# Performance work log

Hardware: AMD Instinct MI355X
Metric: run time of the kernel (lower is better)

The kernel has to match this reference:

```python
import jax, jax.numpy as jnp
import numpy as np

B, T, H, D = 4, 2048, 2048, 4
FF = 4 * H


def _ln(x, s, b):
    m = jnp.mean(x, axis=-1, keepdims=True)
    v = jnp.mean(jnp.square(x - m), axis=-1, keepdims=True)
    return (x - m) * jax.lax.rsqrt(v + 1e-5) * s + b


def setup_inputs() -> dict:
    key = jax.random.key(0)
    ks = jax.random.split(key, 12)
    std = 0.02  # matches nn.init.normal_(std=0.02*(layer_id+1)) with layer_id=0
    # time_decay_multi init: row d filled with 0.9**(d+1)
    td = jnp.repeat((0.9 ** jnp.arange(1, D + 1, dtype=jnp.float32))[:, None], H, axis=1)
    return {
        "x": jax.random.normal(ks[0], (B, T, H), jnp.float32),
        "att_state": jax.random.normal(ks[1], (B, D, H), jnp.float32) * 0.1,
        "cm_state": jax.random.normal(ks[2], (B, H), jnp.float32),
        "ln1_s": jnp.ones((H,), jnp.float32),
        "ln1_b": jnp.zeros((H,), jnp.float32),
        "ln2_s": jnp.ones((H,), jnp.float32),
        "ln2_b": jnp.zeros((H,), jnp.float32),
        "td_multi": td,
        "lvl_w": jax.random.normal(ks[3], (H, D), jnp.float32) * std,
        "lvl_b": jnp.zeros((D,), jnp.float32),
        "Wv": jax.random.normal(ks[4], (H, H), jnp.float32) * std,
        "Wk": jax.random.normal(ks[5], (H, H), jnp.float32) * std,
        "Wr": jax.random.normal(ks[6], (H, H), jnp.float32) * std,
        "Wo": jax.random.normal(ks[7], (H, H), jnp.float32) * std,
        "tmk": jnp.full((H,), 0.5, jnp.float32),
        "Wkey": jax.random.normal(ks[8], (H, FF), jnp.float32) * std,
        "Wval": jax.random.normal(ks[9], (FF, H), jnp.float32) * std,
        "Wgate": jax.random.normal(ks[10], (FF, H), jnp.float32) * std,
    }


def reference(x, att_state, cm_state, ln1_s, ln1_b, ln2_s, ln2_b,
              td_multi, lvl_w, lvl_b, Wv, Wk, Wr, Wo,
              tmk, Wkey, Wval, Wgate):
    # ---- HierarchicalTimeAttention (pre-LN, residual) ----
    h = _ln(x, ln1_s, ln1_b)
    v = h @ Wv                      # [B,T,H]
    k = h @ Wk
    r = jax.nn.sigmoid(h @ Wr)
    lw = jax.nn.softmax(h @ lvl_w + lvl_b, axis=-1)   # [B,T,D]
    decay = jnp.exp(-jnp.exp(td_multi))               # [D,H]
    kv = k * v                                        # [B,T,H]
    # Faithful to source: state is never reassigned inside the time loop,
    # so s[t,d] = state0[d]*decay[d] + k_t*v_t (parallel over t).
    s = att_state[:, None] * decay[None, None] + kv[:, :, None, :]  # [B,T,D,H]
    weighted = jnp.einsum('btd,btdh->bth', lw, s)
    att = (r * weighted) @ Wo
    x1 = x + att
    # ---- RWKVChannelMix (pre-LN, residual, GLU) ----
    h2 = _ln(x1, ln2_s, ln2_b)
    x_mix = jnp.concatenate([cm_state[:, None], h2[:, :-1]], axis=1)  # token shift
    km = h2 * tmk + x_mix * (1.0 - tmk)
    kk = jnp.square(jax.nn.relu(km @ Wkey))           # [B,T,4H]
    out = (kk @ Wval) * jax.nn.sigmoid(kk @ Wgate)    # GLU, ffn_scale=1.0
    return x1 + out
```

## Files before the change

### kernel.cpp

```cpp
#include <hip/hip_runtime.h>


typedef unsigned short u16;
typedef short short8 __attribute__((ext_vector_type(8)));
typedef float f32x4 __attribute__((ext_vector_type(4)));
typedef unsigned short u16x4 __attribute__((ext_vector_type(4)));

#define GAS(p) (const __attribute__((address_space(1))) void*)(p)
#define LAS(p) (__attribute__((address_space(3))) void*)(p)

__device__ __forceinline__ float bf2f(u16 h) { return __uint_as_float(((unsigned)h) << 16); }
__device__ __forceinline__ u16 f2bf(float f) {
  unsigned u = __float_as_uint(f);
  u += 0x7FFFu + ((u >> 16) & 1u);
  return (u16)(u >> 16);
}
__device__ __forceinline__ float sigmoidf_(float x) { return 1.f / (1.f + expf(-x)); }

__global__ __launch_bounds__(256) void transpose_bf16_kernel(
    const float* __restrict__ in, u16* __restrict__ out, int R, int C, int rs, int ro) {
  __shared__ float tile[32][33];
  const int cb = blockIdx.x * 32, rb = blockIdx.y * 32;
  const int tx = threadIdx.x, ty = threadIdx.y;
#pragma unroll
  for (int i = 0; i < 32; i += 8)
    tile[ty + i][tx] = in[(size_t)(rb + ty + i) * C + (cb + tx)];
  __syncthreads();
#pragma unroll
  for (int i = 0; i < 32; i += 8)
    out[((size_t)(cb + ty + i) * rs + ro) * R + (rb + tx)] = f2bf(tile[tx][ty + i]);
}

template <bool WITH_LW>
__global__ __launch_bounds__(256) void ln_kernel(
    const float* __restrict__ x, const float* __restrict__ sc, const float* __restrict__ bi,
    u16* __restrict__ hout,
    const float* __restrict__ lvlw, const float* __restrict__ lvlb,
    float* __restrict__ lwout) {
  const int tid = threadIdx.x;
  const int row = blockIdx.x;
  const int wv = tid >> 6, ln = tid & 63;
  const float* xr = x + (size_t)row * 2048;
  f32x4 a0 = *(const f32x4*)(xr + tid * 4);
  f32x4 a1 = *(const f32x4*)(xr + 1024 + tid * 4);
  float s = a0[0] + a0[1] + a0[2] + a0[3] + a1[0] + a1[1] + a1[2] + a1[3];
  float q = a0[0]*a0[0] + a0[1]*a0[1] + a0[2]*a0[2] + a0[3]*a0[3]
          + a1[0]*a1[0] + a1[1]*a1[1] + a1[2]*a1[2] + a1[3]*a1[3];
#pragma unroll
  for (int off = 32; off; off >>= 1) { s += __shfl_down(s, off); q += __shfl_down(q, off); }
  __shared__ float red[8];
  __shared__ float stats[2];
  if (ln == 0) { red[wv] = s; red[4 + wv] = q; }
  __syncthreads();
  if (tid == 0) {
    float S1 = red[0] + red[1] + red[2] + red[3];
    float S2 = red[4] + red[5] + red[6] + red[7];
    float m = S1 * (1.f / 2048.f);
    float var = S2 * (1.f / 2048.f) - m * m;
    stats[0] = m;
    stats[1] = rsqrtf(var + 1e-5f);
  }
  __syncthreads();
  const float m = stats[0], rs = stats[1];
  f32x4 s0 = *(const f32x4*)(sc + tid * 4), s1 = *(const f32x4*)(sc + 1024 + tid * 4);
  f32x4 b0 = *(const f32x4*)(bi + tid * 4), b1 = *(const f32x4*)(bi + 1024 + tid * 4);
  float h0[4], h1[4];
  u16x4 o0, o1;
#pragma unroll
  for (int e = 0; e < 4; e++) {
    h0[e] = (a0[e] - m) * rs * s0[e] + b0[e];
    h1[e] = (a1[e] - m) * rs * s1[e] + b1[e];
    o0[e] = f2bf(h0[e]);
    o1[e] = f2bf(h1[e]);
  }
  u16* hr = hout + (size_t)row * 2048;
  *(u16x4*)(hr + tid * 4) = o0;
  *(u16x4*)(hr + 1024 + tid * 4) = o1;

  if constexpr (WITH_LW) {
    f32x4 acc = (f32x4){0.f, 0.f, 0.f, 0.f};
#pragma unroll
    for (int e = 0; e < 4; e++)
      acc += (*(const f32x4*)(lvlw + (size_t)(tid * 4 + e) * 4)) * h0[e];
#pragma unroll
    for (int e = 0; e < 4; e++)
      acc += (*(const f32x4*)(lvlw + (size_t)(1024 + tid * 4 + e) * 4)) * h1[e];
#pragma unroll
    for (int off = 32; off; off >>= 1) {
      acc[0] += __shfl_down(acc[0], off);
      acc[1] += __shfl_down(acc[1], off);
      acc[2] += __shfl_down(acc[2], off);
      acc[3] += __shfl_down(acc[3], off);
    }
    __shared__ float red4[16];
    if (ln == 0) {
      red4[wv * 4 + 0] = acc[0]; red4[wv * 4 + 1] = acc[1];
      red4[wv * 4 + 2] = acc[2]; red4[wv * 4 + 3] = acc[3];
    }
    __syncthreads();
    if (tid == 0) {
      float lg[4];
#pragma unroll
      for (int d = 0; d < 4; d++)
        lg[d] = red4[d] + red4[4 + d] + red4[8 + d] + red4[12 + d] + lvlb[d];
      float mx = fmaxf(fmaxf(lg[0], lg[1]), fmaxf(lg[2], lg[3]));
      float e0 = expf(lg[0] - mx), e1 = expf(lg[1] - mx), e2 = expf(lg[2] - mx), e3 = expf(lg[3] - mx);
      float inv = 1.f / (e0 + e1 + e2 + e3);
      float* lr = lwout + (size_t)row * 4;
      lr[0] = e0 * inv; lr[1] = e1 * inv; lr[2] = e2 * inv; lr[3] = e3 * inv;
    }
  }
}

__global__ __launch_bounds__(256) void mix_u_kernel(
    const u16* __restrict__ v, const u16* __restrict__ k, const u16* __restrict__ r,
    const float* __restrict__ lw, const float* __restrict__ att, const float* __restrict__ td,
    u16* __restrict__ u) {
  const size_t i4 = ((size_t)blockIdx.x * 256 + threadIdx.x) * 4;
  const int row = (int)(i4 >> 11);
  const int hh = (int)(i4 & 2047);
  const int b = row >> 11;
  f32x4 lwv = *(const f32x4*)(lw + (size_t)row * 4);
  u16x4 k_ = *(const u16x4*)(k + i4);
  u16x4 v_ = *(const u16x4*)(v + i4);
  u16x4 r_ = *(const u16x4*)(r + i4);
  f32x4 kv, acc = (f32x4){0.f, 0.f, 0.f, 0.f};
#pragma unroll
  for (int e = 0; e < 4; e++) kv[e] = bf2f(k_[e]) * bf2f(v_[e]);
#pragma unroll
  for (int d = 0; d < 4; d++) {
    f32x4 as_ = *(const f32x4*)(att + (size_t)(b * 4 + d) * 2048 + hh);
    f32x4 tdv = *(const f32x4*)(td + (size_t)d * 2048 + hh);
#pragma unroll
    for (int e = 0; e < 4; e++)
      acc[e] += lwv[d] * (as_[e] * expf(-expf(tdv[e])) + kv[e]);
  }
  u16x4 o;
#pragma unroll
  for (int e = 0; e < 4; e++) o[e] = f2bf(bf2f(r_[e]) * acc[e]);
  *(u16x4*)(u + i4) = o;
}

__global__ __launch_bounds__(256) void shift_mix_kernel(
    const u16* __restrict__ h2, const float* __restrict__ cm, const float* __restrict__ tmk,
    u16* __restrict__ km) {
  const size_t i4 = ((size_t)blockIdx.x * 256 + threadIdx.x) * 4;
  const int hh = (int)(i4 & 2047);
  const int row = (int)(i4 >> 11);
  const int b = row >> 11;
  const int t = row & 2047;
  f32x4 tk = *(const f32x4*)(tmk + hh);
  u16x4 cur_ = *(const u16x4*)(h2 + i4);
  f32x4 prev;
  if (t == 0) {
    prev = *(const f32x4*)(cm + (size_t)b * 2048 + hh);
  } else {
    u16x4 p_ = *(const u16x4*)(h2 + i4 - 2048);
#pragma unroll
    for (int e = 0; e < 4; e++) prev[e] = bf2f(p_[e]);
  }
  u16x4 o;
#pragma unroll
  for (int e = 0; e < 4; e++) {
    float c = bf2f(cur_[e]);
    o[e] = f2bf(c * tk[e] + prev[e] * (1.f - tk[e]));
  }
  *(u16x4*)(km + i4) = o;
}

enum { EPI_ADDX = 0, EPI_RELU2, EPI_VKR, EPI_VG };

#define STAGE(srcrow_, hoff_, dbase_, kc_) do {                                   \
    const u16* g_ = (srcrow_) + (kc_);                                            \
    u16* d_ = (dbase_);                                                           \
    __builtin_amdgcn_global_load_lds(GAS(g_ + (size_t)(hoff_) * 2 * rj64), LAS(d_), 16, 0, 0);          \
    __builtin_amdgcn_global_load_lds(GAS(g_ + (size_t)(hoff_) * 2 * rj64 + rj64), LAS(d_ + 4096), 16, 0, 0); \
  } while (0)

template <int EPI>
__global__ __launch_bounds__(512, 2) void gemm256(
    const u16* __restrict__ A, const u16* __restrict__ Bt,
    void* o0, void* o1, void* o2, const float* __restrict__ aux_f,
    int M, int N, int K) {
  __shared__ __align__(16) u16 lds[65536];
  const int tid = threadIdx.x;
  const int wave = tid >> 6, lane = tid & 63;
  const int qd = lane >> 4, l16 = lane & 15;
  const int wm = wave >> 2, wn = wave & 3;
  (void)M;

  const int nbx = gridDim.x;
  const int nwg = nbx * gridDim.y;
  const int lin = blockIdx.y * nbx + blockIdx.x;
  const int cpx = nwg >> 3;
  const int swz = (lin & 7) * cpx + (lin >> 3);
  const int by = swz / nbx, bx = swz - by * nbx;
  const int brow = by << 8, bcol = bx << 8;

  const int r0 = tid >> 3;
  const int cswz = (((tid & 7) ^ (r0 & 7)) << 3);
  const size_t rj64 = (size_t)64 * K;
  const u16* Arow = A + (size_t)(brow + r0) * K + cswz;
  const u16* Brow = Bt + (size_t)(bcol + r0) * K + cswz;
  u16* const dstw = lds + wave * 512;
#define DA(b_, h_) (dstw + (b_) * 32768 + (h_) * 8192)
#define DB(b_, h_) (dstw + (b_) * 32768 + 16384 + (h_) * 8192)

  const int r7 = l16 & 7;
  const int cS0 = ((qd) ^ r7) << 3;
  const int cS1 = ((4 + qd) ^ r7) << 3;
  const u16* ldsA = lds + wm * 8192 + l16 * 64;
  const u16* ldsB = lds + 16384 + (wn >> 1) * 8192 + ((wn & 1) * 64 + l16) * 64;

  f32x4 acc[8][4];
#pragma unroll
  for (int i = 0; i < 8; i++)
#pragma unroll
    for (int n = 0; n < 4; n++) acc[i][n] = (f32x4){0.f, 0.f, 0.f, 0.f};

  STAGE(Arow, 0, DA(0, 0), 0);
  STAGE(Arow, 1, DA(0, 1), 0);
  STAGE(Brow, 0, DB(0, 0), 0);
  STAGE(Brow, 1, DB(0, 1), 0);
  STAGE(Brow, 0, DB(1, 0), 64);
  STAGE(Brow, 1, DB(1, 1), 64);
  asm volatile("s_waitcnt vmcnt(4)" ::: "memory");
  __builtin_amdgcn_s_barrier();

  const int NT = K >> 6;
  for (int t = 0; t < NT; ++t) {
    const int b = t & 1, nb = b ^ 1;
    const int kc1 = (t + 1) << 6, kc2 = (t + 2) << 6;
    const u16* lA = ldsA + b * 32768;
    const u16* lB = ldsB + b * 32768;
    short8 bfr[4][2];
#pragma unroll
    for (int g = 0; g < 4; ++g) {
      if (g == 0) {
#pragma unroll
        for (int n = 0; n < 4; ++n) {
          bfr[n][0] = *(const short8*)(lB + n * 1024 + cS0);
          bfr[n][1] = *(const short8*)(lB + n * 1024 + cS1);
        }
      }
      short8 af[2][2];
#pragma unroll
      for (int mm = 0; mm < 2; ++mm) {
        af[mm][0] = *(const short8*)(lA + (g * 2 + mm) * 1024 + cS0);
        af[mm][1] = *(const short8*)(lA + (g * 2 + mm) * 1024 + cS1);
      }
      if (g == 0) { if (t + 1 < NT) STAGE(Arow, 0, DA(nb, 0), kc1); }
      else if (g == 1) { if (t + 1 < NT) STAGE(Arow, 1, DA(nb, 1), kc1); }
      else if (g == 2) { if (t + 2 < NT) STAGE(Brow, 0, DB(b, 0), kc2); }
      else             { if (t + 2 < NT) STAGE(Brow, 1, DB(b, 1), kc2); }
      __builtin_amdgcn_s_barrier();
      asm volatile("s_waitcnt lgkmcnt(0)" ::: "memory");
      __builtin_amdgcn_sched_barrier(0);
      __builtin_amdgcn_s_setprio(1);
#pragma unroll
      for (int mm = 0; mm < 2; ++mm)
#pragma unroll
        for (int n = 0; n < 4; ++n)
#pragma unroll
          for (int s = 0; s < 2; ++s)
            acc[g * 2 + mm][n] = __builtin_amdgcn_mfma_f32_16x16x32_bf16(
                af[mm][s], bfr[n][s], acc[g * 2 + mm][n], 0, 0, 0);
      __builtin_amdgcn_s_setprio(0);
      if (g == 3) {
        if (t < NT - 2) asm volatile("s_waitcnt vmcnt(4)" ::: "memory");
        else            asm volatile("s_waitcnt vmcnt(0)" ::: "memory");
      }
      __builtin_amdgcn_s_barrier();
    }
  }

  const int rw = brow + wm * 128 + qd * 4;
  const int cw = bcol + wn * 64 + l16;
#pragma unroll
  for (int i = 0; i < 8; ++i)
#pragma unroll
    for (int n = 0; n < 4; ++n)
#pragma unroll
      for (int rg = 0; rg < 4; ++rg) {
        const int rr = rw + i * 16 + rg;
        const int cc = cw + n * 16;
        const float vv = acc[i][n][rg];
        if constexpr (EPI == EPI_ADDX) {
          const size_t idx = (size_t)rr * N + cc;
          ((float*)o0)[idx] = vv + aux_f[idx];
        } else if constexpr (EPI == EPI_RELU2) {
          const size_t idx = (size_t)rr * N + cc;
          float tt = vv > 0.f ? vv : 0.f;
          ((u16*)o0)[idx] = f2bf(tt * tt);
        } else if constexpr (EPI == EPI_VKR) {
          const int seg = cc >> 11, local = cc & 2047;
          const size_t idx = (size_t)rr * 2048 + local;
          if (seg == 0)      ((u16*)o0)[idx] = f2bf(vv);
          else if (seg == 1) ((u16*)o1)[idx] = f2bf(vv);
          else               ((u16*)o2)[idx] = f2bf(sigmoidf_(vv));
        } else {
          const float part = __shfl_xor(vv, 1);
          if ((l16 & 1) == 0) {
            const size_t idx = (size_t)rr * 2048 + (size_t)(cc >> 1);
            ((float*)o0)[idx] = aux_f[idx] + vv * sigmoidf_(part);
          }
        }
      }
#undef DA
#undef DB
}

extern "C" void kernel_launch(void* const* d_in, const int* in_sizes, int n_in,
                              void* d_out, int out_size, void* d_ws, size_t ws_size,
                              hipStream_t stream) {
  const float* x = (const float*)d_in[0];
  const float* att_state = (const float*)d_in[1];
  const float* cm_state = (const float*)d_in[2];
  const float* ln1_s = (const float*)d_in[3];
  const float* ln1_b = (const float*)d_in[4];
  const float* ln2_s = (const float*)d_in[5];
  const float* ln2_b = (const float*)d_in[6];
  const float* td = (const float*)d_in[7];
  const float* lvl_w = (const float*)d_in[8];
  const float* lvl_b = (const float*)d_in[9];
  const float* Wv = (const float*)d_in[10];
  const float* Wk = (const float*)d_in[11];
  const float* Wr = (const float*)d_in[12];
  const float* Wo = (const float*)d_in[13];
  const float* tmk = (const float*)d_in[14];
  const float* Wkey = (const float*)d_in[15];
  const float* Wval = (const float*)d_in[16];
  const float* Wgate = (const float*)d_in[17];
  float* out = (float*)d_out;

  const size_t S = 8192ull * 2048ull;
  const size_t S4 = 8192ull * 8192ull;
  char* ws = (char*)d_ws;
  u16* bufW = (u16*)(ws);
  u16* hbuf = (u16*)(ws + 1 * S * 2);
  u16* vbuf = (u16*)(ws + 2 * S * 2);
  u16* kbuf = (u16*)(ws + 3 * S * 2);
  u16* rbuf = (u16*)(ws + 4 * S * 2);
  u16* bufVG = hbuf;
  u16* kkbuf = (u16*)(ws + 5 * S * 2);
  float* lwbuf = (float*)(ws + 5 * S * 2 + S4 * 2);
  (void)in_sizes; (void)n_in; (void)out_size; (void)ws_size;

  const dim3 tb256(256);
  const dim3 tb512(512);
  const dim3 ttb(32, 8);
  const dim3 gT2k(64, 64);
  const dim3 gTkey(256, 64);
  const dim3 gTvg(64, 256);
  const dim3 gemm_vkr(6144 / 256, 32);
  const dim3 gemm_wo(2048 / 256, 32);
  const dim3 gemm_kk(8192 / 256, 32);
  const dim3 gemm_vg(4096 / 256, 32);
  const int elemBlocks = (int)(S / 1024);

  ln_kernel<true><<<8192, tb256, 0, stream>>>(x, ln1_s, ln1_b, hbuf, lvl_w, lvl_b, lwbuf);
  transpose_bf16_kernel<<<gT2k, ttb, 0, stream>>>(Wv, bufW, 2048, 2048, 1, 0);
  transpose_bf16_kernel<<<gT2k, ttb, 0, stream>>>(Wk, bufW, 2048, 2048, 1, 2048);
  transpose_bf16_kernel<<<gT2k, ttb, 0, stream>>>(Wr, bufW, 2048, 2048, 1, 4096);
  gemm256<EPI_VKR><<<gemm_vkr, tb512, 0, stream>>>(hbuf, bufW, vbuf, kbuf, rbuf, nullptr, 8192, 6144, 2048);
  mix_u_kernel<<<elemBlocks, tb256, 0, stream>>>(vbuf, kbuf, rbuf, lwbuf, att_state, td, hbuf);
  transpose_bf16_kernel<<<gT2k, ttb, 0, stream>>>(Wo, bufW, 2048, 2048, 1, 0);
  gemm256<EPI_ADDX><<<gemm_wo, tb512, 0, stream>>>(hbuf, bufW, out, nullptr, nullptr, x, 8192, 2048, 2048);
  ln_kernel<false><<<8192, tb256, 0, stream>>>(out, ln2_s, ln2_b, vbuf, nullptr, nullptr, nullptr);
  shift_mix_kernel<<<elemBlocks, tb256, 0, stream>>>(vbuf, cm_state, tmk, kbuf);
  transpose_bf16_kernel<<<gTkey, ttb, 0, stream>>>(Wkey, bufW, 2048, 8192, 1, 0);
  gemm256<EPI_RELU2><<<gemm_kk, tb512, 0, stream>>>(kbuf, bufW, kkbuf, nullptr, nullptr, nullptr, 8192, 8192, 2048);
  transpose_bf16_kernel<<<gTvg, ttb, 0, stream>>>(Wval, bufVG, 8192, 2048, 2, 0);
  transpose_bf16_kernel<<<gTvg, ttb, 0, stream>>>(Wgate, bufVG, 8192, 2048, 2, 1);
  gemm256<EPI_VG><<<gemm_vg, tb512, 0, stream>>>(kkbuf, bufVG, out, nullptr, nullptr, out, 8192, 4096, 8192);
}
```

Baseline: 1.483 ms.

## Restructure GEMM main loop into two half-phases with fewer barriers

Replaces the four sub-phase inner loop (one barrier pair per sub-phase) with two larger phases per K tile. Each phase loads four A fragments and runs 32 MFMAs, so only two barriers remain per tile. Global staging of A is issued before the first barrier and staging of B after it. This cuts synchronisation overhead and gives longer MFMA runs, at the cost of more live fragment registers and coarser interleaving of global loads with compute.

```diff
diff --git a/kernel.cpp b/kernel.cpp
--- a/kernel.cpp
+++ b/kernel.cpp
@@ -233,45 +233,52 @@
     const int kc1 = (t + 1) << 6, kc2 = (t + 2) << 6;
     const u16* lA = ldsA + b * 32768;
     const u16* lB = ldsB + b * 32768;
-    short8 bfr[4][2];
-#pragma unroll
-    for (int g = 0; g < 4; ++g) {
-      if (g == 0) {
-#pragma unroll
-        for (int n = 0; n < 4; ++n) {
-          bfr[n][0] = *(const short8*)(lB + n * 1024 + cS0);
-          bfr[n][1] = *(const short8*)(lB + n * 1024 + cS1);
-        }
-      }
-      short8 af[2][2];
-#pragma unroll
-      for (int mm = 0; mm < 2; ++mm) {
-        af[mm][0] = *(const short8*)(lA + (g * 2 + mm) * 1024 + cS0);
-        af[mm][1] = *(const short8*)(lA + (g * 2 + mm) * 1024 + cS1);
-      }
-      if (g == 0) { if (t + 1 < NT) STAGE(Arow, 0, DA(nb, 0), kc1); }
-      else if (g == 1) { if (t + 1 < NT) STAGE(Arow, 1, DA(nb, 1), kc1); }
-      else if (g == 2) { if (t + 2 < NT) STAGE(Brow, 0, DB(b, 0), kc2); }
-      else             { if (t + 2 < NT) STAGE(Brow, 1, DB(b, 1), kc2); }
-      __builtin_amdgcn_s_barrier();
-      asm volatile("s_waitcnt lgkmcnt(0)" ::: "memory");
-      __builtin_amdgcn_sched_barrier(0);
-      __builtin_amdgcn_s_setprio(1);
-#pragma unroll
-      for (int mm = 0; mm < 2; ++mm)
+    short8 af[4][2], bfr[4][2];
+#pragma unroll
+    for (int i = 0; i < 4; ++i) {
+      af[i][0] = *(const short8*)(lA + i * 1024 + cS0);
+      af[i][1] = *(const short8*)(lA + i * 1024 + cS1);
+    }
+#pragma unroll
+    for (int n = 0; n < 4; ++n) {
+      bfr[n][0] = *(const short8*)(lB + n * 1024 + cS0);
+      bfr[n][1] = *(const short8*)(lB + n * 1024 + cS1);
+    }
+    if (t + 1 < NT) { STAGE(Arow, 0, DA(nb, 0), kc1); STAGE(Arow, 1, DA(nb, 1), kc1); }
+    asm volatile("s_waitcnt lgkmcnt(0)" ::: "memory");
+    __builtin_amdgcn_sched_barrier(0);
+    __builtin_amdgcn_s_barrier();
+    if (t + 2 < NT) { STAGE(Brow, 0, DB(b, 0), kc2); STAGE(Brow, 1, DB(b, 1), kc2); }
+    __builtin_amdgcn_s_setprio(1);
+#pragma unroll
+    for (int s = 0; s < 2; ++s)
+#pragma unroll
+      for (int i = 0; i < 4; ++i)
 #pragma unroll
         for (int n = 0; n < 4; ++n)
-#pragma unroll
-          for (int s = 0; s < 2; ++s)
-            acc[g * 2 + mm][n] = __builtin_amdgcn_mfma_f32_16x16x32_bf16(
-                af[mm][s], bfr[n][s], acc[g * 2 + mm][n], 0, 0, 0);
-      __builtin_amdgcn_s_setprio(0);
-      if (g == 3) {
-        if (t < NT - 2) asm volatile("s_waitcnt vmcnt(4)" ::: "memory");
-        else            asm volatile("s_waitcnt vmcnt(0)" ::: "memory");
-      }
-      __builtin_amdgcn_s_barrier();
-    }
+          acc[i][n] = __builtin_amdgcn_mfma_f32_16x16x32_bf16(
+              af[i][s], bfr[n][s], acc[i][n], 0, 0, 0);
+    __builtin_amdgcn_s_setprio(0);
+#pragma unroll
+    for (int i = 0; i < 4; ++i) {
+      af[i][0] = *(const short8*)(lA + (4 + i) * 1024 + cS0);
+      af[i][1] = *(const short8*)(lA + (4 + i) * 1024 + cS1);
+    }
+    asm volatile("s_waitcnt lgkmcnt(0)" ::: "memory");
+    __builtin_amdgcn_sched_barrier(0);
+    __builtin_amdgcn_s_setprio(1);
+#pragma unroll
+    for (int s = 0; s < 2; ++s)
+#pragma unroll
+      for (int i = 0; i < 4; ++i)
+#pragma unroll
+        for (int n = 0; n < 4; ++n)
+          acc[4 + i][n] = __builtin_amdgcn_mfma_f32_16x16x32_bf16(
+              af[i][s], bfr[n][s], acc[4 + i][n], 0, 0, 0);
+    __builtin_amdgcn_s_setprio(0);
+    if (t < NT - 2) asm volatile("s_waitcnt vmcnt(4)" ::: "memory");
+    else            asm volatile("s_waitcnt vmcnt(0)" ::: "memory");
+    __builtin_amdgcn_s_barrier();
   }
 
   const int rw = brow + wm * 128 + qd * 4;
```

Measured after the change: 1.517 ms. 2.2% more time.
